# Optimization experiments

Measured on AMD Instinct MI355X. Metric: run time of the kernel, lower is better.

Reference implementation:

```python
import jax, jax.numpy as jnp
import numpy as np


def setup_inputs() -> dict:
    key = jax.random.key(0)
    k1, k2, k3, k4 = jax.random.split(key, 4)
    B, IN, OUT, K = 1024, 1024, 1024, 100
    return {
        "x": jax.random.normal(k1, (B, IN), dtype=jnp.float32),
        "eps": jax.random.normal(k2, (K, IN, OUT), dtype=jnp.float32),
        "weights_m": jax.random.normal(k3, (IN, OUT), dtype=jnp.float32),
        "weights_s": jax.random.normal(k4, (IN, OUT), dtype=jnp.float32),
    }


def reference(x, eps, weights_m, weights_s):
    # Reparameterized Gaussian weight samples: [K, in, out]
    sampled = eps * jax.nn.softplus(weights_s) + weights_m
    # einsum('ij,kjl->kil'): preds [K, B, out]
    preds = jnp.einsum('ij,kjl->kil', x, sampled)
    return preds.mean(0)
```

## Files before the change

### kernel.cpp

```cpp
#include <hip/hip_runtime.h>
#include <cmath>

#define KSAMP 100
#define DIN   1024
#define DOUT  1024
#define DB    1024

__global__ __launch_bounds__(256) void weff_kernel(
    const float4* __restrict__ eps,
    const float4* __restrict__ wm,
    const float4* __restrict__ ws,
    float4* __restrict__ weff)
{
    const int idx = blockIdx.x * blockDim.x + threadIdx.x;
    const int n4 = (DIN * DOUT) / 4;

    float sx = 0.f, sy = 0.f, sz = 0.f, sw = 0.f;
    const float4* p = eps + idx;
    #pragma unroll 4
    for (int k = 0; k < KSAMP; ++k) {
        float4 e = p[(size_t)k * n4];
        sx += e.x; sy += e.y; sz += e.z; sw += e.w;
    }

    float4 s = ws[idx];
    float4 m = wm[idx];
    const float invK = 1.0f / (float)KSAMP;

    float spx = fmaxf(s.x, 0.f) + log1pf(expf(-fabsf(s.x)));
    float spy = fmaxf(s.y, 0.f) + log1pf(expf(-fabsf(s.y)));
    float spz = fmaxf(s.z, 0.f) + log1pf(expf(-fabsf(s.z)));
    float spw = fmaxf(s.w, 0.f) + log1pf(expf(-fabsf(s.w)));

    float4 o;
    o.x = fmaf(sx * invK, spx, m.x);
    o.y = fmaf(sy * invK, spy, m.y);
    o.z = fmaf(sz * invK, spz, m.z);
    o.w = fmaf(sw * invK, spw, m.w);
    weff[idx] = o;
}

#define BM 128
#define BN 128
#define BK 8
#define KSPLIT 4

__global__ __launch_bounds__(256) void sgemm_splitk(
    const float* __restrict__ A,
    const float* __restrict__ B,
    float* __restrict__ C)
{
    __shared__ float As[BK][BM];
    __shared__ float Bs[BK][BN];

    const int bx = blockIdx.x, by = blockIdx.y, kz = blockIdx.z;
    const int tid = threadIdx.x;
    const int tx = tid & 15;
    const int ty = tid >> 4;

    const int kc = DIN / KSPLIT;
    const int k_begin = kz * kc;
    const int k_end   = k_begin + kc;

    const int arow = tid >> 1;
    const int acol = (tid & 1) * 4;
    const int brow = tid >> 5;
    const int bcol = (tid & 31) * 4;

    float acc[8][8];
    #pragma unroll
    for (int i = 0; i < 8; ++i)
        #pragma unroll
        for (int j = 0; j < 8; ++j) acc[i][j] = 0.f;

    for (int k0 = k_begin; k0 < k_end; k0 += BK) {
        float4 a = *(const float4*)&A[(size_t)(by * BM + arow) * DIN + k0 + acol];
        float4 b = *(const float4*)&B[(size_t)(k0 + brow) * DOUT + bx * BN + bcol];

        __syncthreads();
        As[acol + 0][arow] = a.x;
        As[acol + 1][arow] = a.y;
        As[acol + 2][arow] = a.z;
        As[acol + 3][arow] = a.w;
        *(float4*)&Bs[brow][bcol] = b;
        __syncthreads();

        #pragma unroll
        for (int kk = 0; kk < BK; ++kk) {
            float4 a0 = *(const float4*)&As[kk][ty * 8];
            float4 a1 = *(const float4*)&As[kk][ty * 8 + 4];
            float4 b0 = *(const float4*)&Bs[kk][tx * 8];
            float4 b1 = *(const float4*)&Bs[kk][tx * 8 + 4];
            const float ar[8] = {a0.x, a0.y, a0.z, a0.w, a1.x, a1.y, a1.z, a1.w};
            const float br[8] = {b0.x, b0.y, b0.z, b0.w, b1.x, b1.y, b1.z, b1.w};
            #pragma unroll
            for (int i = 0; i < 8; ++i)
                #pragma unroll
                for (int j = 0; j < 8; ++j)
                    acc[i][j] = fmaf(ar[i], br[j], acc[i][j]);
        }
    }

    #pragma unroll
    for (int i = 0; i < 8; ++i) {
        const int r = by * BM + ty * 8 + i;
        float* crow = &C[(size_t)r * DOUT + bx * BN + tx * 8];
        #pragma unroll
        for (int j = 0; j < 8; ++j)
            atomicAdd(&crow[j], acc[i][j]);
    }
}

extern "C" void kernel_launch(void* const* d_in, const int* in_sizes, int n_in,
                              void* d_out, int out_size, void* d_ws, size_t ws_size,
                              hipStream_t stream) {
    const float* x   = (const float*)d_in[0];
    const float* eps = (const float*)d_in[1];
    const float* wm  = (const float*)d_in[2];
    const float* ws  = (const float*)d_in[3];
    float* out  = (float*)d_out;
    float* weff = (float*)d_ws;

    hipMemsetAsync(d_out, 0, (size_t)out_size * sizeof(float), stream);

    weff_kernel<<<(DIN * DOUT / 4) / 256, 256, 0, stream>>>(
        (const float4*)eps, (const float4*)wm, (const float4*)ws, (float4*)weff);

    sgemm_splitk<<<dim3(DOUT / BN, DB / BM, KSPLIT), 256, 0, stream>>>(x, weff, out);
}
```

Before: 711.2 us.

## Replace atomic split-K with partial buffers and reduction; nontemporal eps loads; prefetch GEMM tiles

The eps-mean kernel now uses vector-typed nontemporal loads with two independent accumulators and a larger unroll, so more loads are in flight while streaming the 400MB tensor. The GEMM split-K factor doubles to 8, gets a launch-bounds occupancy hint, and prefetches the next global tile into registers during compute. Per-slice partials are written to workspace with plain vector stores and summed by a separate reduce kernel, replacing the memset plus atomics. This costs extra workspace and an extra kernel launch with its own memory traffic.

```diff
diff --git a/kernel.cpp b/kernel.cpp
--- a/kernel.cpp
+++ b/kernel.cpp
@@ -6,49 +6,57 @@
 #define DOUT  1024
 #define DB    1024
 
+typedef float f4 __attribute__((ext_vector_type(4)));
+
 __global__ __launch_bounds__(256) void weff_kernel(
-    const float4* __restrict__ eps,
-    const float4* __restrict__ wm,
-    const float4* __restrict__ ws,
-    float4* __restrict__ weff)
+    const f4* __restrict__ eps,
+    const f4* __restrict__ wm,
+    const f4* __restrict__ ws,
+    f4* __restrict__ weff)
 {
     const int idx = blockIdx.x * blockDim.x + threadIdx.x;
     const int n4 = (DIN * DOUT) / 4;
 
-    float sx = 0.f, sy = 0.f, sz = 0.f, sw = 0.f;
-    const float4* p = eps + idx;
-    #pragma unroll 4
-    for (int k = 0; k < KSAMP; ++k) {
-        float4 e = p[(size_t)k * n4];
-        sx += e.x; sy += e.y; sz += e.z; sw += e.w;
+    f4 acc0 = {0.f, 0.f, 0.f, 0.f};
+    f4 acc1 = {0.f, 0.f, 0.f, 0.f};
+    const f4* p = eps + idx;
+    #pragma unroll 10
+    for (int k = 0; k < KSAMP; k += 2) {
+        f4 e0 = __builtin_nontemporal_load(p);
+        f4 e1 = __builtin_nontemporal_load(p + n4);
+        p += 2 * n4;
+        acc0 += e0;
+        acc1 += e1;
     }
+    f4 sum = acc0 + acc1;
 
-    float4 s = ws[idx];
-    float4 m = wm[idx];
+    f4 s = ws[idx];
+    f4 m = wm[idx];
     const float invK = 1.0f / (float)KSAMP;
 
-    float spx = fmaxf(s.x, 0.f) + log1pf(expf(-fabsf(s.x)));
-    float spy = fmaxf(s.y, 0.f) + log1pf(expf(-fabsf(s.y)));
-    float spz = fmaxf(s.z, 0.f) + log1pf(expf(-fabsf(s.z)));
-    float spw = fmaxf(s.w, 0.f) + log1pf(expf(-fabsf(s.w)));
+    f4 sp;
+    sp.x = fmaxf(s.x, 0.f) + log1pf(expf(-fabsf(s.x)));
+    sp.y = fmaxf(s.y, 0.f) + log1pf(expf(-fabsf(s.y)));
+    sp.z = fmaxf(s.z, 0.f) + log1pf(expf(-fabsf(s.z)));
+    sp.w = fmaxf(s.w, 0.f) + log1pf(expf(-fabsf(s.w)));
 
-    float4 o;
-    o.x = fmaf(sx * invK, spx, m.x);
-    o.y = fmaf(sy * invK, spy, m.y);
-    o.z = fmaf(sz * invK, spz, m.z);
-    o.w = fmaf(sw * invK, spw, m.w);
+    f4 o;
+    o.x = fmaf(sum.x * invK, sp.x, m.x);
+    o.y = fmaf(sum.y * invK, sp.y, m.y);
+    o.z = fmaf(sum.z * invK, sp.z, m.z);
+    o.w = fmaf(sum.w * invK, sp.w, m.w);
     weff[idx] = o;
 }
 
 #define BM 128
 #define BN 128
 #define BK 8
-#define KSPLIT 4
+#define KSPLIT 8
 
-__global__ __launch_bounds__(256) void sgemm_splitk(
+__global__ __launch_bounds__(256, 2) void sgemm_splitk(
     const float* __restrict__ A,
     const float* __restrict__ B,
-    float* __restrict__ C)
+    float* __restrict__ P)
 {
     __shared__ float As[BK][BM];
     __shared__ float Bs[BK][BN];
@@ -60,12 +68,14 @@
 
     const int kc = DIN / KSPLIT;
     const int k_begin = kz * kc;
-    const int k_end   = k_begin + kc;
 
     const int arow = tid >> 1;
     const int acol = (tid & 1) * 4;
     const int brow = tid >> 5;
     const int bcol = (tid & 31) * 4;
+
+    const float* Aptr = &A[(size_t)(by * BM + arow) * DIN + k_begin + acol];
+    const float* Bptr = &B[(size_t)(k_begin + brow) * DOUT + bx * BN + bcol];
 
     float acc[8][8];
     #pragma unroll
@@ -73,10 +83,11 @@
         #pragma unroll
         for (int j = 0; j < 8; ++j) acc[i][j] = 0.f;
 
-    for (int k0 = k_begin; k0 < k_end; k0 += BK) {
-        float4 a = *(const float4*)&A[(size_t)(by * BM + arow) * DIN + k0 + acol];
-        float4 b = *(const float4*)&B[(size_t)(k0 + brow) * DOUT + bx * BN + bcol];
+    float4 a = *(const float4*)Aptr;
+    float4 b = *(const float4*)Bptr;
 
+    const int niter = kc / BK;
+    for (int it = 0; it < niter; ++it) {
         __syncthreads();
         As[acol + 0][arow] = a.x;
         As[acol + 1][arow] = a.y;
@@ -84,6 +95,11 @@
         As[acol + 3][arow] = a.w;
         *(float4*)&Bs[brow][bcol] = b;
         __syncthreads();
+
+        if (it + 1 < niter) {
+            a = *(const float4*)(Aptr + (it + 1) * BK);
+            b = *(const float4*)(Bptr + (size_t)(it + 1) * BK * DOUT);
+        }
 
         #pragma unroll
         for (int kk = 0; kk < BK; ++kk) {
@@ -101,14 +117,27 @@
         }
     }
 
+    float* Pz = P + (size_t)kz * DB * DOUT;
     #pragma unroll
     for (int i = 0; i < 8; ++i) {
         const int r = by * BM + ty * 8 + i;
-        float* crow = &C[(size_t)r * DOUT + bx * BN + tx * 8];
-        #pragma unroll
-        for (int j = 0; j < 8; ++j)
-            atomicAdd(&crow[j], acc[i][j]);
+        float* prow = &Pz[(size_t)r * DOUT + bx * BN + tx * 8];
+        *(float4*)&prow[0] = make_float4(acc[i][0], acc[i][1], acc[i][2], acc[i][3]);
+        *(float4*)&prow[4] = make_float4(acc[i][4], acc[i][5], acc[i][6], acc[i][7]);
     }
+}
+
+__global__ __launch_bounds__(256) void reduce_kernel(
+    const f4* __restrict__ P, f4* __restrict__ out)
+{
+    const int idx = blockIdx.x * blockDim.x + threadIdx.x;
+    const int n4 = (DB * DOUT) / 4;
+    f4 s = P[idx];
+    #pragma unroll
+    for (int z = 1; z < KSPLIT; ++z) {
+        s += P[(size_t)z * n4 + idx];
+    }
+    out[idx] = s;
 }
 
 extern "C" void kernel_launch(void* const* d_in, const int* in_sizes, int n_in,
@@ -118,13 +147,16 @@
     const float* eps = (const float*)d_in[1];
     const float* wm  = (const float*)d_in[2];
     const float* ws  = (const float*)d_in[3];
-    float* out  = (float*)d_out;
-    float* weff = (float*)d_ws;
 
-    hipMemsetAsync(d_out, 0, (size_t)out_size * sizeof(float), stream);
+    float* weff     = (float*)d_ws;
+    float* partials = (float*)d_ws + (size_t)DIN * DOUT;
 
     weff_kernel<<<(DIN * DOUT / 4) / 256, 256, 0, stream>>>(
-        (const float4*)eps, (const float4*)wm, (const float4*)ws, (float4*)weff);
+        (const f4*)eps, (const f4*)wm, (const f4*)ws, (f4*)weff);
 
-    sgemm_splitk<<<dim3(DOUT / BN, DB / BM, KSPLIT), 256, 0, stream>>>(x, weff, out);
+    sgemm_splitk<<<dim3(DOUT / BN, DB / BM, KSPLIT), 256, 0, stream>>>(
+        x, weff, partials);
+
+    reduce_kernel<<<(DB * DOUT / 4) / 256, 256, 0, stream>>>(
+        (const f4*)partials, (f4*)d_out);
 }
```

New measurement: 580.8 us. -18.3%, faster.
